# Kernel optimization log

Hardware: AMD Instinct MI355X
Metric: run time of the kernel (lower is better)

The kernel has to match this reference:

```python
import jax, jax.numpy as jnp
import numpy as np


def setup_inputs() -> dict:
    key = jax.random.key(0)
    ks = jax.random.split(key, 8)
    B, S, A = 128, 256, 128   # rows, seq, channels
    H, KD, VD, O = 8, 16, 16, 128
    w_scale = 1.0 / np.sqrt(A)
    return {
        "q_data": jax.random.normal(ks[0], (B, S, A), jnp.float32),
        "bias": jax.random.normal(ks[1], (B, S, S), jnp.float32),
        "nonbatched_bias": jax.random.normal(ks[2], (S, S), jnp.float32),
        "query_w": jax.random.normal(ks[3], (A, H, KD), jnp.float32) * w_scale,
        "key_w": jax.random.normal(ks[4], (A, H, KD), jnp.float32) * w_scale,
        "value_w": jax.random.normal(ks[5], (A, H, VD), jnp.float32) * w_scale,
        "gating_w": jax.random.normal(ks[6], (A, H, VD), jnp.float32) * w_scale,
        "output_w": jax.random.normal(ks[7], (H, VD, O), jnp.float32) * w_scale,
    }


def reference(q_data, bias, nonbatched_bias, query_w, key_w, value_w, gating_w, output_w):
    # Gated multihead self-attention (AlphaFold grid self-attention).
    key_dim = query_w.shape[-1]
    scale = key_dim ** -0.5
    # fused QKV + gate projections from q_data (self-attention: m_data == q_data)
    q = jnp.einsum('bqa,ahc->bqhc', q_data, query_w) * scale
    k = jnp.einsum('bka,ahc->bkhc', q_data, key_w)
    v = jnp.einsum('bka,ahc->bkhc', q_data, value_w)
    # logits [B, H, Q, K] + batched bias + shared nonbatched bias
    logits = (jnp.einsum('bqhc,bkhc->bhqk', q, k)
              + bias[:, None, :, :]
              + nonbatched_bias[None, None, :, :])
    weights = jax.nn.softmax(logits, axis=-1)
    weighted_avg = jnp.einsum('bhqk,bkhc->bqhc', weights, v)
    gate = jax.nn.sigmoid(jnp.einsum('bqa,ahc->bqhc', q_data, gating_w))
    out = jnp.einsum('bqhc,hco->bqo', gate * weighted_avg, output_w)
    return out
```

## Files before the change

kernel.cpp:

```cpp
#include <hip/hip_runtime.h>
#include <math.h>

#define BB 128
#define SS 256
#define AA 128
#define HH 8
#define CC 16
#define HCC 128
#define OO 128

typedef float f32x4 __attribute__((ext_vector_type(4)));
typedef short s16x4 __attribute__((ext_vector_type(4)));
typedef unsigned short u16x4 __attribute__((ext_vector_type(4)));

__device__ __forceinline__ unsigned bf16_rne(float x) {
    union { float f; unsigned u; } v; v.f = x;
    return (v.u + 0x7fffu + ((v.u >> 16) & 1u)) >> 16;
}
__device__ __forceinline__ unsigned pack_bf16(float lo, float hi) {
    return bf16_rne(lo) | (bf16_rne(hi) << 16);
}

__device__ __forceinline__ void mfma16(f32x4& d, s16x4 a, s16x4 b) {
#if __has_builtin(__builtin_amdgcn_mfma_f32_16x16x16bf16_1k)
    d = __builtin_amdgcn_mfma_f32_16x16x16bf16_1k(a, b, d, 0, 0, 0);
#else
    asm("v_mfma_f32_16x16x16_bf16 %0, %1, %2, %0" : "+v"(d) : "v"(a), "v"(b));
#endif
}

__global__ __launch_bounds__(256) void prep_w_kernel(
    const float* __restrict__ wq, const float* __restrict__ wk,
    const float* __restrict__ wv, const float* __restrict__ wg,
    const float* __restrict__ wo, unsigned short* __restrict__ wt16)
{
    const int j = blockIdx.x >> 4;
    const int t = ((blockIdx.x & 15) << 8) + threadIdx.x;
    const float* W = (j == 0) ? wq : (j == 1) ? wk : (j == 2) ? wv
                   : (j == 3) ? wg : wo;
    const int outch = t >> 5;
    const int a0 = (t & 31) * 4;
    u16x4 v;
    #pragma unroll
    for (int u = 0; u < 4; ++u)
        v[u] = (unsigned short)bf16_rne(W[(size_t)(a0 + u) * 128 + outch]);
    *(u16x4*)((char*)wt16 + (size_t)j * 32768 + outch * 256
              + ((a0 * 2) ^ ((outch & 7) << 5))) = v;
}

__global__ __launch_bounds__(512, 2) void qkvg_mfma_kernel(
    const float* __restrict__ qdata, const unsigned short* __restrict__ wt16,
    unsigned short* __restrict__ qb, unsigned short* __restrict__ kb,
    unsigned short* __restrict__ vtb, float* __restrict__ g_ws)
{
    __shared__ char wlds[65536];
    const int tid = threadIdx.x;
    const int w = tid >> 6;
    const int lane = tid & 63;
    const int lo = lane & 15, gg = lane >> 4;
    const int sb = blockIdx.x * 128;
    const int s = sb + w * 16 + lo;
    const int b = sb >> 8;
    const int srow = (sb & 255) + w * 16;
    const int m0 = blockIdx.y * 2;

    {
        const uint4* src = (const uint4*)(wt16 + (size_t)m0 * 16384);
        uint4* dst = (uint4*)wlds;
        #pragma unroll
        for (int i = 0; i < 8; ++i) dst[i * 512 + tid] = src[i * 512 + tid];
    }

    s16x4 qd[8];
    {
        const float* qp = qdata + (size_t)s * AA;
        #pragma unroll
        for (int t = 0; t < 8; ++t) {
            float4 f = *(const float4*)(qp + t * 16 + gg * 4);
            unsigned w0 = pack_bf16(f.x, f.y), w1 = pack_bf16(f.z, f.w);
            s16x4 q; ((unsigned*)&q)[0] = w0; ((unsigned*)&q)[1] = w1;
            qd[t] = q;
        }
    }
    __syncthreads();

    for (int mi = 0; mi < 2; ++mi) {
        const int m = m0 + mi;
        const char* wbase = wlds + mi * 32768;
        #pragma unroll
        for (int cf = 0; cf < 8; ++cf) {
            s16x4 wf[8];
            #pragma unroll
            for (int t = 0; t < 8; ++t) {
                int boff = (cf * 16 + lo) * 256 + ((t * 32 + gg * 8) ^ ((lo & 7) << 5));
                wf[t] = *(const s16x4*)(wbase + boff);
            }
            f32x4 acc = {0.f, 0.f, 0.f, 0.f};
            if (m == 2) {
                #pragma unroll
                for (int t = 0; t < 8; ++t) mfma16(acc, qd[t], wf[t]);
                u16x4 o;
                #pragma unroll
                for (int r = 0; r < 4; ++r) o[r] = (unsigned short)bf16_rne(acc[r]);
                *(u16x4*)(vtb + (((size_t)b * HH + cf) * CC + lo) * SS
                          + srow + gg * 4) = o;
            } else {
                #pragma unroll
                for (int t = 0; t < 8; ++t) mfma16(acc, wf[t], qd[t]);
                if (m == 0) {
                    u16x4 o;
                    #pragma unroll
                    for (int r = 0; r < 4; ++r)
                        o[r] = (unsigned short)bf16_rne(acc[r] * 0.25f);
                    *(u16x4*)(qb + (((size_t)b * HH + cf) * SS + srow + lo) * CC
                              + gg * 4) = o;
                } else if (m == 1) {
                    u16x4 o;
                    #pragma unroll
                    for (int r = 0; r < 4; ++r) o[r] = (unsigned short)bf16_rne(acc[r]);
                    *(u16x4*)(kb + (((size_t)b * HH + cf) * SS + srow + lo) * CC
                              + gg * 4) = o;
                } else {
                    float4 g;
                    g.x = 1.f / (1.f + __expf(-acc[0]));
                    g.y = 1.f / (1.f + __expf(-acc[1]));
                    g.z = 1.f / (1.f + __expf(-acc[2]));
                    g.w = 1.f / (1.f + __expf(-acc[3]));
                    *(float4*)(g_ws + ((size_t)b * SS + srow + lo) * HCC
                               + cf * 16 + gg * 4) = g;
                }
            }
        }
    }
}

__global__ __launch_bounds__(512, 2) void attn_fused_kernel(
    const unsigned short* __restrict__ qb,
    const unsigned short* __restrict__ kb,
    const unsigned short* __restrict__ vtb,
    const float* __restrict__ g_ws,
    const float* __restrict__ bias,
    const float* __restrict__ nb,
    const unsigned short* __restrict__ wo16,
    float* __restrict__ out)
{
    __shared__ char smem[65536];
    const int tid = threadIdx.x;
    const int blk = blockIdx.x;
    const int b = blk >> 2;
    const int Q0 = (blk & 3) * 64;

    {
        const float4* bsrc = (const float4*)(bias + ((size_t)b * SS + Q0) * SS);
        const float4* nsrc = (const float4*)(nb + (size_t)Q0 * SS);
        #pragma unroll
        for (int i = 0; i < 8; ++i) {
            int idx = i * 512 + tid;
            int r = idx >> 6, c4 = idx & 63;
            float4 bv = bsrc[idx];
            float4 nv = nsrc[idx];
            bv.x += nv.x; bv.y += nv.y; bv.z += nv.z; bv.w += nv.w;
            int byteoff = r * 1024 + ((c4 * 16) ^ ((r & 7) << 4));
            *(float4*)(smem + byteoff) = bv;
        }
    }
    __syncthreads();

    const int wv = tid >> 6;
    const int lane = tid & 63;
    const int lo = lane & 15, gg = lane >> 4;
    const size_t bh = (size_t)b * HH + wv;

    s16x4 kf[16], vf[16];
    {
        const unsigned short* kp = kb + bh * SS * CC;
        const unsigned short* vp = vtb + bh * CC * SS;
        #pragma unroll
        for (int t = 0; t < 16; ++t)
            kf[t] = *(const s16x4*)(kp + (t * 16 + lo) * CC + gg * 4);
        #pragma unroll
        for (int t = 0; t < 16; ++t)
            vf[t] = *(const s16x4*)(vp + lo * SS + t * 16 + gg * 4);
    }
    const unsigned short* qp = qb + bh * SS * CC;

    f32x4 ov[4];
    for (int qt = 0; qt < 4; ++qt) {
        const int qrow = Q0 + qt * 16 + lo;
        s16x4 qf = *(const s16x4*)(qp + qrow * CC + gg * 4);
        const int rl = qt * 16 + lo;
        f32x4 S[16];
        #pragma unroll
        for (int t = 0; t < 16; ++t) {
            int byteoff = rl * 1024 + (((t * 4 + gg) * 16) ^ ((rl & 7) << 4));
            S[t] = *(const f32x4*)(smem + byteoff);
        }
        #pragma unroll
        for (int t = 0; t < 16; ++t) mfma16(S[t], kf[t], qf);
        asm volatile("s_nop 7\n\ts_nop 7");

        float lsum = 0.f;
        unsigned pw[32];
        #pragma unroll
        for (int t = 0; t < 16; ++t) {
            float p0 = __expf(S[t][0] - 12.f), p1 = __expf(S[t][1] - 12.f);
            float p2 = __expf(S[t][2] - 12.f), p3 = __expf(S[t][3] - 12.f);
            lsum += (p0 + p1) + (p2 + p3);
            pw[t * 2]     = pack_bf16(p0, p1);
            pw[t * 2 + 1] = pack_bf16(p2, p3);
        }
        lsum += __shfl_xor(lsum, 16);
        lsum += __shfl_xor(lsum, 32);

        f32x4 W0 = {0.f, 0.f, 0.f, 0.f}, W1 = {0.f, 0.f, 0.f, 0.f};
        asm volatile("s_nop 7");
        #pragma unroll
        for (int t = 0; t < 16; t += 2) {
            s16x4 pa; ((unsigned*)&pa)[0] = pw[t * 2];     ((unsigned*)&pa)[1] = pw[t * 2 + 1];
            mfma16(W0, vf[t], pa);
            s16x4 pb; ((unsigned*)&pb)[0] = pw[t * 2 + 2]; ((unsigned*)&pb)[1] = pw[t * 2 + 3];
            mfma16(W1, vf[t + 1], pb);
        }
        asm volatile("s_nop 7\n\ts_nop 7");

        const float inv = 1.f / lsum;
        float4 gt = *(const float4*)(g_ws + ((size_t)b * SS + qrow) * HCC
                                     + wv * 16 + gg * 4);
        f32x4 o;
        o[0] = (W0[0] + W1[0]) * inv * gt.x;
        o[1] = (W0[1] + W1[1]) * inv * gt.y;
        o[2] = (W0[2] + W1[2]) * inv * gt.z;
        o[3] = (W0[3] + W1[3]) * inv * gt.w;
        ov[qt] = o;
    }

    __syncthreads();
    {
        #pragma unroll
        for (int qt = 0; qt < 4; ++qt) {
            int rl = qt * 16 + lo;
            uint2 pk;
            pk.x = pack_bf16(ov[qt][0], ov[qt][1]);
            pk.y = pack_bf16(ov[qt][2], ov[qt][3]);
            int byteoff = rl * 256 + ((wv * 32 + gg * 8) ^ ((rl & 7) << 4));
            *(uint2*)(smem + byteoff) = pk;
        }
        const uint4* src = (const uint4*)wo16;
        uint4* dst = (uint4*)(smem + 16384);
        #pragma unroll
        for (int i = 0; i < 4; ++i) dst[i * 512 + tid] = src[i * 512 + tid];
    }
    __syncthreads();

    {
        const int rt = wv & 3;
        const int ob = (wv >> 2) * 4;
        const int r = rt * 16 + lo;
        #pragma unroll
        for (int oi = 0; oi < 4; ++oi) {
            const int ot = ob + oi;
            f32x4 acc = {0.f, 0.f, 0.f, 0.f};
            #pragma unroll
            for (int kt = 0; kt < 8; ++kt) {
                s16x4 wf = *(const s16x4*)(smem + 16384 + (ot * 16 + lo) * 256
                             + ((kt * 32 + gg * 8) ^ ((lo & 7) << 5)));
                s16x4 gb = *(const s16x4*)(smem + r * 256
                             + ((kt * 32 + gg * 8) ^ ((r & 7) << 4)));
                mfma16(acc, wf, gb);
            }
            float4 o4; o4.x = acc[0]; o4.y = acc[1]; o4.z = acc[2]; o4.w = acc[3];
            *(float4*)(out + ((size_t)b * SS + Q0 + rt * 16 + lo) * OO
                       + ot * 16 + gg * 4) = o4;
        }
    }
}

extern "C" void kernel_launch(void* const* d_in, const int* in_sizes, int n_in,
                              void* d_out, int out_size, void* d_ws, size_t ws_size,
                              hipStream_t stream) {
    const float* qdata = (const float*)d_in[0];
    const float* bias  = (const float*)d_in[1];
    const float* nb    = (const float*)d_in[2];
    const float* wq    = (const float*)d_in[3];
    const float* wk    = (const float*)d_in[4];
    const float* wv    = (const float*)d_in[5];
    const float* wg    = (const float*)d_in[6];
    const float* wo    = (const float*)d_in[7];
    float* out = (float*)d_out;

    const size_t QKV = (size_t)BB * HH * SS * CC;
    unsigned short* qb   = (unsigned short*)d_ws;
    unsigned short* kbp  = qb + QKV;
    unsigned short* vtb  = kbp + QKV;
    unsigned short* wt16 = vtb + QKV;
    float* g_ws = (float*)(wt16 + 5 * 16384);

    prep_w_kernel<<<dim3(80), dim3(256), 0, stream>>>(wq, wk, wv, wg, wo, wt16);
    qkvg_mfma_kernel<<<dim3((BB * SS) / 128, 2), dim3(512), 0, stream>>>(
        qdata, wt16, qb, kbp, vtb, g_ws);
    attn_fused_kernel<<<dim3(BB * 4), dim3(512), 0, stream>>>(
        qb, kbp, vtb, g_ws, bias, nb, wt16 + 4 * 16384, out);
}
```

Baseline: 148.8 us.

## Fold weight bf16 conversion into consumer kernels and widen bias LDS swizzle

```diff
diff --git a/kernel.cpp b/kernel.cpp
--- a/kernel.cpp
+++ b/kernel.cpp
@@ -29,27 +29,28 @@
 #endif
 }
 
-__global__ __launch_bounds__(256) void prep_w_kernel(
+__device__ __forceinline__ void stage_weight_16(
+    const float* __restrict__ W, char* base, int a00, int lane)
+{
+    #pragma unroll
+    for (int a4 = 0; a4 < 4; ++a4) {
+        const int a0 = a00 + a4 * 4;
+        #pragma unroll
+        for (int oh = 0; oh < 2; ++oh) {
+            const int oc = oh * 64 + lane;
+            u16x4 pk;
+            #pragma unroll
+            for (int j = 0; j < 4; ++j)
+                pk[j] = (unsigned short)bf16_rne(W[(size_t)(a0 + j) * 128 + oc]);
+            *(u16x4*)(base + oc * 256 + ((a0 * 2) ^ ((oc & 7) << 5))) = pk;
+        }
+    }
+}
+
+__global__ __launch_bounds__(512, 2) void qkvg_mfma_kernel(
+    const float* __restrict__ qdata,
     const float* __restrict__ wq, const float* __restrict__ wk,
     const float* __restrict__ wv, const float* __restrict__ wg,
-    const float* __restrict__ wo, unsigned short* __restrict__ wt16)
-{
-    const int j = blockIdx.x >> 4;
-    const int t = ((blockIdx.x & 15) << 8) + threadIdx.x;
-    const float* W = (j == 0) ? wq : (j == 1) ? wk : (j == 2) ? wv
-                   : (j == 3) ? wg : wo;
-    const int outch = t >> 5;
-    const int a0 = (t & 31) * 4;
-    u16x4 v;
-    #pragma unroll
-    for (int u = 0; u < 4; ++u)
-        v[u] = (unsigned short)bf16_rne(W[(size_t)(a0 + u) * 128 + outch]);
-    *(u16x4*)((char*)wt16 + (size_t)j * 32768 + outch * 256
-              + ((a0 * 2) ^ ((outch & 7) << 5))) = v;
-}
-
-__global__ __launch_bounds__(512, 2) void qkvg_mfma_kernel(
-    const float* __restrict__ qdata, const unsigned short* __restrict__ wt16,
     unsigned short* __restrict__ qb, unsigned short* __restrict__ kb,
     unsigned short* __restrict__ vtb, float* __restrict__ g_ws)
 {
@@ -65,10 +66,12 @@
     const int m0 = blockIdx.y * 2;
 
     {
-        const uint4* src = (const uint4*)(wt16 + (size_t)m0 * 16384);
-        uint4* dst = (uint4*)wlds;
-        #pragma unroll
-        for (int i = 0; i < 8; ++i) dst[i * 512 + tid] = src[i * 512 + tid];
+        const float* Wm = (w < 4) ? ((m0 == 0) ? wq : wv)
+                                  : ((m0 == 0) ? wk : wg);
+        char* base = wlds + (w >> 2) * 32768;
+        const int a00 = (w & 3) * 32;
+        stage_weight_16(Wm, base, a00,      lane);
+        stage_weight_16(Wm, base, a00 + 16, lane);
     }
 
     s16x4 qd[8];
@@ -141,7 +144,7 @@
     const float* __restrict__ g_ws,
     const float* __restrict__ bias,
     const float* __restrict__ nb,
-    const unsigned short* __restrict__ wo16,
+    const float* __restrict__ wo,
     float* __restrict__ out)
 {
     __shared__ char smem[65536];
@@ -160,7 +163,7 @@
             float4 bv = bsrc[idx];
             float4 nv = nsrc[idx];
             bv.x += nv.x; bv.y += nv.y; bv.z += nv.z; bv.w += nv.w;
-            int byteoff = r * 1024 + ((c4 * 16) ^ ((r & 7) << 4));
+            int byteoff = r * 1024 + ((c4 * 16) ^ ((r & 15) << 4));
             *(float4*)(smem + byteoff) = bv;
         }
     }
@@ -192,7 +195,7 @@
         f32x4 S[16];
         #pragma unroll
         for (int t = 0; t < 16; ++t) {
-            int byteoff = rl * 1024 + (((t * 4 + gg) * 16) ^ ((rl & 7) << 4));
+            int byteoff = rl * 1024 + (((t * 4 + gg) * 16) ^ ((rl & 15) << 4));
             S[t] = *(const f32x4*)(smem + byteoff);
         }
         #pragma unroll
@@ -245,10 +248,7 @@
             int byteoff = rl * 256 + ((wv * 32 + gg * 8) ^ ((rl & 7) << 4));
             *(uint2*)(smem + byteoff) = pk;
         }
-        const uint4* src = (const uint4*)wo16;
-        uint4* dst = (uint4*)(smem + 16384);
-        #pragma unroll
-        for (int i = 0; i < 4; ++i) dst[i * 512 + tid] = src[i * 512 + tid];
+        stage_weight_16(wo, smem + 16384, wv * 16, lane);
     }
     __syncthreads();
 
@@ -289,15 +289,13 @@
     float* out = (float*)d_out;
 
     const size_t QKV = (size_t)BB * HH * SS * CC;
-    unsigned short* qb   = (unsigned short*)d_ws;
-    unsigned short* kbp  = qb + QKV;
-    unsigned short* vtb  = kbp + QKV;
-    unsigned short* wt16 = vtb + QKV;
-    float* g_ws = (float*)(wt16 + 5 * 16384);
-
-    prep_w_kernel<<<dim3(80), dim3(256), 0, stream>>>(wq, wk, wv, wg, wo, wt16);
+    unsigned short* qb  = (unsigned short*)d_ws;
+    unsigned short* kbp = qb + QKV;
+    unsigned short* vtb = kbp + QKV;
+    float* g_ws = (float*)(vtb + QKV);
+
     qkvg_mfma_kernel<<<dim3((BB * SS) / 128, 2), dim3(512), 0, stream>>>(
-        qdata, wt16, qb, kbp, vtb, g_ws);
+        qdata, wq, wk, wv, wg, qb, kbp, vtb, g_ws);
     attn_fused_kernel<<<dim3(BB * 4), dim3(512), 0, stream>>>(
-        qb, kbp, vtb, g_ws, bias, nb, wt16 + 4 * 16384, out);
-}
+        qb, kbp, vtb, g_ws, bias, nb, wo, out);
+}
```

After: 148.9 us. About the same (+0.1%).
